# Optimization experiments

Hardware: AMD Instinct MI355X
Metric: run time of the kernel (lower is better)

The kernel has to match this reference:

```python
import jax, jax.numpy as jnp
import numpy as np

DIM = 320
D_STATE = 32
D_CONV = 4
EXPAND = 2
HEADDIM = 80
D_INNER = EXPAND * DIM          # 640
NHEADS = D_INNER // HEADDIM     # 8
NGROUPS = 1
CONV_DIM = D_INNER + 2 * NGROUPS * D_STATE          # 704
D_IN_PROJ = 2 * D_INNER + 2 * NGROUPS * D_STATE + NHEADS  # 1352
PATCH = (16, 16, 16)
NUM_PT_EMB = 2


def setup_inputs() -> dict:
    key = jax.random.key(0)
    ks = jax.random.split(key, 16)
    B, Np = 4, 8
    x = jax.random.normal(ks[0], (B, DIM) + PATCH, dtype=jnp.float32)
    point_coords = jax.random.uniform(ks[1], (B, Np, 3), dtype=jnp.float32) * jnp.asarray(PATCH, jnp.float32)
    point_labels = jax.random.randint(ks[2], (B, Np), 0, 2)
    return {
        "x": x,
        "point_coords": point_coords,
        "ln_w": jnp.ones((DIM,), jnp.float32),
        "ln_b": jnp.zeros((DIM,), jnp.float32),
        "in_proj_w": jax.random.normal(ks[3], (D_IN_PROJ, DIM), jnp.float32) * 0.02,
        "conv_w": jax.random.normal(ks[4], (CONV_DIM, 1, D_CONV), jnp.float32) * 0.2,
        "conv_b": jax.random.normal(ks[5], (CONV_DIM,), jnp.float32) * 0.02,
        "dt_bias": jax.random.uniform(ks[6], (NHEADS,), jnp.float32, 0.0, 0.1),
        "A_log": jnp.log(jax.random.uniform(ks[7], (NHEADS,), jnp.float32, 1.0, 16.0)),
        "Dp": jnp.ones((NHEADS,), jnp.float32),
        "rms_w": jnp.ones((D_INNER,), jnp.float32),
        "out_proj_w": jax.random.normal(ks[8], (DIM, D_INNER), jnp.float32) * 0.02,
        "pe_gauss": jax.random.normal(ks[9], (3, DIM // 2), jnp.float32),
        "point_embed": jax.random.normal(ks[10], (NUM_PT_EMB, DIM), jnp.float32) * 0.02,
        "not_a_point": jax.random.normal(ks[11], (DIM,), jnp.float32) * 0.02,
        "point_labels": point_labels,
    }


def _forward(x, point_coords, ln_w, ln_b, in_proj_w, conv_w, conv_b, dt_bias,
             A_log, Dp, rms_w, out_proj_w, pe_gauss, point_embed, not_a_point,
             point_labels):
    B, C = x.shape[:2]
    img_dims = x.shape[2:]
    n_tokens = int(np.prod(img_dims))
    xf = x.reshape(B, C, n_tokens).transpose(0, 2, 1)  # (B, T, C)

    # ---- PointEncoder (SAM-style random Fourier positional embedding) ----
    pc = point_coords / jnp.asarray(PATCH, x.dtype)     # normalize to [0,1]
    pc = 2.0 * pc - 1.0
    pe = (2.0 * jnp.pi) * (pc @ pe_gauss)               # (B, Np, DIM/2)
    pemb = jnp.concatenate([jnp.sin(pe), jnp.cos(pe)], axis=-1)  # (B, Np, DIM)
    lbl = point_labels[..., None]
    safe = jnp.clip(point_labels, 0, NUM_PT_EMB - 1)
    pemb = jnp.where(lbl == -1, not_a_point, pemb + point_embed[safe])

    seq = jnp.concatenate([xf, pemb], axis=1)           # (B, L, C)
    L = seq.shape[1]

    # ---- LayerNorm ----
    mu = seq.mean(-1, keepdims=True)
    var = jnp.mean((seq - mu) ** 2, axis=-1, keepdims=True)
    xn = (seq - mu) * jax.lax.rsqrt(var + 1e-5) * ln_w + ln_b

    # ---- Mamba2 ----
    zxbcdt = xn @ in_proj_w.T                            # (B, L, 1352)
    z = zxbcdt[..., :D_INNER]
    xBC = zxbcdt[..., D_INNER:D_INNER + CONV_DIM]
    dt = zxbcdt[..., D_INNER + CONV_DIM:]                # (B, L, H)
    dt = jax.nn.softplus(dt + dt_bias)

    # causal depthwise conv1d over channels
    conv = jax.lax.conv_general_dilated(
        xBC.transpose(0, 2, 1), conv_w, (1,), [(D_CONV - 1, 0)],
        feature_group_count=CONV_DIM,
        dimension_numbers=("NCH", "OIH", "NCH"))
    xBC = jax.nn.silu((conv + conv_b[None, :, None]).transpose(0, 2, 1))

    xs = xBC[..., :D_INNER].reshape(B, L, NHEADS, HEADDIM)
    Bm = xBC[..., D_INNER:D_INNER + D_STATE]             # (B, L, N), ngroups=1
    Cm = xBC[..., D_INNER + D_STATE:]                    # (B, L, N)

    A = -jnp.exp(A_log)                                  # (H,)
    dA = jnp.exp(dt * A)                                 # (B, L, H)

    def step(h, inp):
        dA_t, dt_t, B_t, C_t, x_t = inp
        h = h * dA_t[:, :, None, None] + jnp.einsum('bh,bn,bhp->bhpn', dt_t, B_t, x_t)
        y = jnp.einsum('bhpn,bn->bhp', h, C_t)
        return h, y

    inps = (dA.transpose(1, 0, 2), dt.transpose(1, 0, 2),
            Bm.transpose(1, 0, 2), Cm.transpose(1, 0, 2),
            xs.transpose(1, 0, 2, 3))
    h0 = jnp.zeros((B, NHEADS, HEADDIM, D_STATE), x.dtype)
    _, ys = jax.lax.scan(step, h0, inps)                 # (L, B, H, P)
    y = ys.transpose(1, 0, 2, 3) + xs * Dp[None, None, :, None]
    y = y.reshape(B, L, D_INNER)

    # gated RMSNorm
    y = y * jax.nn.silu(z)
    y = y * jax.lax.rsqrt(jnp.mean(y * y, axis=-1, keepdims=True) + 1e-5) * rms_w
    out = y @ out_proj_w.T                               # (B, L, DIM)

    out = out[:, :n_tokens].transpose(0, 2, 1).reshape(B, C, *img_dims)
    return out


def reference(x, point_coords, ln_w, ln_b, in_proj_w, conv_w, conv_b, dt_bias,
              A_log, Dp, rms_w, out_proj_w, pe_gauss, point_embed, not_a_point,
              point_labels):
    return _forward(x, point_coords, ln_w, ln_b, in_proj_w, conv_w, conv_b,
                    dt_bias, A_log, Dp, rms_w, out_proj_w, pe_gauss,
                    point_embed, not_a_point, point_labels)
```

## Files before the change

kernel.cpp:

```cpp
#include <hip/hip_runtime.h>
#include <math.h>

#define BQ 4
#define LQ 4104
#define NTQ 4096
#define CDIM 320
#define DIP 1352
#define DI 640
#define CONVD 704
#define NH 8
#define HD 80
#define DS 32
#define MQ (BQ*LQ)
#define QC 64
#define NC 65

typedef __attribute__((ext_vector_type(8))) short bf16x8;
typedef __attribute__((ext_vector_type(4))) float f32x4;

__device__ __forceinline__ unsigned short f2bf(float f){
  union { float f; unsigned u; } v; v.f = f;
  unsigned r = v.u + 0x7FFFu + ((v.u >> 16) & 1u);
  return (unsigned short)(r >> 16);
}
__device__ __forceinline__ float bf2f(unsigned short u){
  union { unsigned u; float f; } v; v.u = ((unsigned)u) << 16;
  return v.f;
}
__device__ __forceinline__ float warp_sum(float v){
  #pragma unroll
  for (int o = 32; o; o >>= 1) v += __shfl_xor(v, o);
  return v;
}
__device__ __forceinline__ void gload16(const unsigned short* g, unsigned short* l){
  __builtin_amdgcn_global_load_lds(
      (const __attribute__((address_space(1))) unsigned int*)g,
      (__attribute__((address_space(3))) unsigned int*)l, 16, 0, 0);
}
__device__ __forceinline__ int swz64(int p, int i){
  return p*QC + (i ^ ((p & 7) << 3));
}

__global__ __launch_bounds__(256) void k_f2bf2(
    const float* __restrict__ s1, unsigned short* __restrict__ d1, int n1,
    const float* __restrict__ s2, unsigned short* __restrict__ d2, int n2)
{
  int i = blockIdx.x*256 + threadIdx.x;
  if (i < n1) d1[i] = f2bf(s1[i]);
  else if (i - n1 < n2) d2[i - n1] = f2bf(s2[i - n1]);
}

__global__ __launch_bounds__(256) void k_zero(float* __restrict__ p, int n)
{
  int i = blockIdx.x*256 + threadIdx.x;
  if (i < n) p[i] = 0.f;
}

__global__ __launch_bounds__(256) void k_stats(
    const float* __restrict__ x, float* __restrict__ muS, float* __restrict__ s2S)
{
  int b = blockIdx.z;
  int cs0 = blockIdx.y * 40;
  int tok = blockIdx.x*256 + threadIdx.x;
  const float* xb = x + ((size_t)b*CDIM)*NTQ;
  float s = 0.f, s2 = 0.f;
  #pragma unroll 8
  for (int c = cs0; c < cs0 + 40; c++) {
    float v = xb[(size_t)c*NTQ + tok];
    s += v; s2 = fmaf(v, v, s2);
  }
  atomicAdd(&muS[b*NTQ + tok], s);
  atomicAdd(&s2S[b*NTQ + tok], s2);
}

__global__ __launch_bounds__(256) void k_norm_t(
    const float* __restrict__ x, const float* __restrict__ muS,
    const float* __restrict__ s2S, const float* __restrict__ lnw,
    const float* __restrict__ lnb, unsigned short* __restrict__ xnh)
{
  int b = blockIdx.z;
  int c0 = blockIdx.y * 64;
  int t0 = blockIdx.x * 64;
  int t = threadIdx.x;
  int lt = t & 63, cg = t >> 6;
  const float* xb = x + ((size_t)b*CDIM)*NTQ;

  __shared__ unsigned short T[64][72];
  __shared__ float muL[64], rsL[64];
  if (t < 64) {
    float s  = muS[b*NTQ + t0 + t];
    float s2 = s2S[b*NTQ + t0 + t];
    float mu = s*(1.0f/CDIM);
    muL[t] = mu;
    rsL[t] = rsqrtf(s2*(1.0f/CDIM) - mu*mu + 1e-5f);
  }
  __syncthreads();
  float mu = muL[lt], rs = rsL[lt];
  #pragma unroll
  for (int c = cg; c < 64; c += 4) {
    float v = xb[(size_t)(c0+c)*NTQ + t0 + lt];
    T[lt][c] = f2bf((v - mu)*rs*lnw[c0+c] + lnb[c0+c]);
  }
  __syncthreads();
  #pragma unroll
  for (int i = 0; i < 4; i++) {
    int idx = t + 256*i;
    int tok = idx >> 4, cq = idx & 15;
    *(uint2*)&xnh[((size_t)(b*LQ) + t0 + tok)*CDIM + c0 + cq*4] =
        *(const uint2*)&T[tok][cq*4];
  }
}

__global__ __launch_bounds__(320) void k_pt_ln(
    const float* __restrict__ pcoords, const float* __restrict__ lnw,
    const float* __restrict__ lnb, const float* __restrict__ pgauss,
    const float* __restrict__ pemb_w, const float* __restrict__ nap,
    const int* __restrict__ plabels, unsigned short* __restrict__ xnh)
{
  int j = blockIdx.x, b = blockIdx.y;
  int c = threadIdx.x;
  int f = (c < 160) ? c : c - 160;
  float p0 = pcoords[(b*8+j)*3+0]*(2.0f/16.0f) - 1.0f;
  float p1 = pcoords[(b*8+j)*3+1]*(2.0f/16.0f) - 1.0f;
  float p2 = pcoords[(b*8+j)*3+2]*(2.0f/16.0f) - 1.0f;
  float pe = 6.283185307179586f*(p0*pgauss[f] + p1*pgauss[160+f] + p2*pgauss[320+f]);
  float pv = (c < 160) ? sinf(pe) : cosf(pe);
  int lab = plabels[b*8+j];
  float val;
  if (lab == -1) val = nap[c];
  else {
    int safe = lab < 0 ? 0 : (lab > 1 ? 1 : lab);
    val = pv + pemb_w[safe*CDIM + c];
  }
  float s  = warp_sum(val);
  float s2 = warp_sum(val*val);
  __shared__ float r1[5], r2[5];
  int w = threadIdx.x >> 6, lane = threadIdx.x & 63;
  if (lane == 0) { r1[w] = s; r2[w] = s2; }
  __syncthreads();
  float ts = 0.f, ts2 = 0.f;
  #pragma unroll
  for (int i = 0; i < 5; i++) { ts += r1[i]; ts2 += r2[i]; }
  float mu  = ts * (1.0f/CDIM);
  float var = ts2 * (1.0f/CDIM) - mu*mu;
  float rsig = rsqrtf(var + 1e-5f);
  xnh[((size_t)b*LQ + NTQ + j)*CDIM + c] = f2bf((val - mu)*rsig*lnw[c] + lnb[c]);
}

__global__ __launch_bounds__(256) void k_gemm1_mfma(
    const unsigned short* __restrict__ Abf, const unsigned short* __restrict__ Wbf,
    unsigned short* __restrict__ zxh, float* __restrict__ dtraw)
{
  __shared__ unsigned short As[128*32];
  __shared__ unsigned short Bs[128*32];
  int id = blockIdx.x;
  int xcd = id & 7, pos = id >> 3;
  const int q = 177, r = 3;
  int swz = (xcd < r ? xcd*(q+1) : r*(q+1) + (xcd-r)*q) + pos;
  int m0 = (swz / 11) * 128;
  int n0 = (swz % 11) * 128;
  int tid = threadIdx.x;
  int lane = tid & 63, wid = tid >> 6;
  int wr = wid >> 1, wc = wid & 1;
  int fr = lane & 15, fq = lane >> 4;

  int srow = lane >> 2;
  int scol = (lane & 3) * 8;

  f32x4 acc[4][4] = {};
  for (int k0 = 0; k0 < CDIM; k0 += 32) {
    #pragma unroll
    for (int i = 0; i < 2; i++) {
      int seg = wid + i*4;
      int rowA = seg*16 + srow;
      int ga = m0 + rowA; if (ga > MQ-1) ga = MQ-1;
      gload16(Abf + (size_t)ga*CDIM + k0 + scol, &As[seg*512]);
      int gb = n0 + rowA; if (gb > DIP-1) gb = DIP-1;
      gload16(Wbf + (size_t)gb*CDIM + k0 + scol, &Bs[seg*512]);
    }
    __syncthreads();
    bf16x8 fa[4], fb[4];
    #pragma unroll
    for (int i = 0; i < 4; i++) {
      fa[i] = *(const bf16x8*)&As[(wr*64 + i*16 + fr)*32 + fq*8];
      fb[i] = *(const bf16x8*)&Bs[(wc*64 + i*16 + fr)*32 + fq*8];
    }
    #pragma unroll
    for (int i = 0; i < 4; i++)
      #pragma unroll
      for (int j = 0; j < 4; j++)
        acc[i][j] = __builtin_amdgcn_mfma_f32_16x16x32_bf16(fa[i], fb[j], acc[i][j], 0, 0, 0);
    __syncthreads();
  }
  #pragma unroll
  for (int i = 0; i < 4; i++) {
    #pragma unroll
    for (int j = 0; j < 4; j++) {
      #pragma unroll
      for (int rr = 0; rr < 4; rr++) {
        int grow = m0 + wr*64 + i*16 + fq*4 + rr;
        int gcol = n0 + wc*64 + j*16 + fr;
        if (grow < MQ && gcol < DIP) {
          float v = acc[i][j][rr];
          zxh[(size_t)grow*DIP + gcol] = f2bf(v);
          if (gcol >= DI + CONVD)
            dtraw[(size_t)grow*NH + (gcol - (DI + CONVD))] = v;
        }
      }
    }
  }
}

__global__ __launch_bounds__(256) void k_conv(
    const unsigned short* __restrict__ zxh, const float* __restrict__ cw,
    const float* __restrict__ cb, unsigned short* __restrict__ xcb)
{
  const int nC4 = CONVD/4;
  int gid = blockIdx.x*256 + threadIdx.x;
  if (gid >= (MQ/8)*nC4) return;
  int c4 = gid % nC4;
  int mb = gid / nC4;
  int m0 = mb*8;
  int l0 = m0 % LQ;
  int c0 = c4*4;
  float4 cbv = *(const float4*)(cb + c0);
  float4 w0 = *(const float4*)(cw + (c0+0)*4);
  float4 w1 = *(const float4*)(cw + (c0+1)*4);
  float4 w2 = *(const float4*)(cw + (c0+2)*4);
  float4 w3 = *(const float4*)(cw + (c0+3)*4);
  const float* wp[4] = {(const float*)&w0, (const float*)&w1,
                        (const float*)&w2, (const float*)&w3};
  float vals[11][4];
  #pragma unroll
  for (int r = 0; r < 11; r++) {
    int ls = l0 - 3 + r;
    uint2 u = make_uint2(0,0);
    if (ls >= 0)
      u = *(const uint2*)(zxh + (size_t)(m0-3+r)*DIP + DI + c0);
    vals[r][0] = bf2f((unsigned short)(u.x & 0xffff));
    vals[r][1] = bf2f((unsigned short)(u.x >> 16));
    vals[r][2] = bf2f((unsigned short)(u.y & 0xffff));
    vals[r][3] = bf2f((unsigned short)(u.y >> 16));
  }
  const float* cbp = (const float*)&cbv;
  #pragma unroll
  for (int u = 0; u < 8; u++) {
    unsigned short o[4];
    #pragma unroll
    for (int ch = 0; ch < 4; ch++) {
      float a = cbp[ch];
      #pragma unroll
      for (int j = 0; j < 4; j++)
        a = fmaf(vals[u+j][ch], wp[ch][j], a);
      o[ch] = f2bf(a / (1.f + __expf(-a)));
    }
    *(uint2*)(xcb + (size_t)(m0+u)*CONVD + c0) = *(const uint2*)o;
  }
}

__global__ __launch_bounds__(256) void k_cumsum_state(
    const float* __restrict__ dtraw, const float* __restrict__ dt_bias,
    const float* __restrict__ A_log, const unsigned short* __restrict__ xcb,
    float* __restrict__ dtb, float* __restrict__ cs, float* __restrict__ Dc,
    float* __restrict__ Sbuf)
{
  int c = blockIdx.x, h = blockIdx.y, b = blockIdx.z;
  int len = LQ - c*QC; if (len > QC) len = QC;
  int t = threadIdx.x;
  int lane = t & 63, wid = t >> 6;
  int fr = lane & 15, fq = lane >> 4;
  int m0 = b*LQ + c*QC;

  __shared__ unsigned short XT[HD*QC];
  __shared__ unsigned short BwT[DS*QC];
  __shared__ float sm[QC], dtl[QC], ws[QC];

  for (int idx = t; idx < (HD/8)*QC; idx += 256) {
    int pg = idx % 10, i = idx / 10;
    uint4 v = make_uint4(0,0,0,0);
    if (i < len)
      v = *(const uint4*)(xcb + (size_t)(m0+i)*CONVD + h*HD + pg*8);
    union { uint4 u; unsigned short us[8]; } cv; cv.u = v;
    #pragma unroll
    for (int e = 0; e < 8; e++)
      XT[swz64(pg*8+e, i)] = cv.us[e];
  }

  float A = -expf(A_log[h]);
  if (t < QC) {
    float sp = 0.f;
    if (t < len) {
      float v = dtraw[((size_t)(m0+t))*NH + h] + dt_bias[h];
      sp = (v > 20.f) ? v : log1pf(expf(v));
      dtb[((size_t)(m0+t))*NH + h] = sp;
    }
    dtl[t] = sp;
    sm[t] = sp * A;
  }
  __syncthreads();
  for (int off = 1; off < QC; off <<= 1) {
    float v = 0.f;
    if (t < QC && t >= off) v = sm[t-off];
    __syncthreads();
    if (t < QC) sm[t] += v;
    __syncthreads();
  }
  if (t < QC) cs[((size_t)(b*NH+h)*NC + c)*QC + t] = sm[t];
  if (t == len-1) Dc[(b*NH+h)*NC + c] = expf(sm[t]);
  if (t < QC) ws[t] = (t < len) ? __expf(sm[len-1] - sm[t]) * dtl[t] : 0.f;
  __syncthreads();
  for (int idx = t; idx < DS*QC; idx += 256) {
    int n = idx & 31, i = idx >> 5;
    float v = (i < len) ? bf2f(xcb[(size_t)(m0+i)*CONVD + DI + n]) * ws[i] : 0.f;
    BwT[swz64(n, i)] = f2bf(v);
  }
  __syncthreads();

  size_t base = ((size_t)(b*NC + c)*NH + h)*(HD*DS);
  for (int tp = wid; tp < 10; tp += 4) {
    int pi = tp >> 1, ni = tp & 1;
    f32x4 acc = {};
    #pragma unroll
    for (int ks = 0; ks < 2; ks++) {
      bf16x8 fa = *(const bf16x8*)&XT[swz64(pi*16 + fr, ks*32 + fq*8)];
      bf16x8 fb = *(const bf16x8*)&BwT[swz64(ni*16 + fr, ks*32 + fq*8)];
      acc = __builtin_amdgcn_mfma_f32_16x16x32_bf16(fa, fb, acc, 0, 0, 0);
    }
    #pragma unroll
    for (int rr = 0; rr < 4; rr++)
      Sbuf[base + (size_t)(pi*16 + fq*4 + rr)*DS + ni*16 + fr] = acc[rr];
  }
}

__global__ __launch_bounds__(256) void k_state_scan(
    float* __restrict__ Sbuf, const float* __restrict__ Dc,
    float* __restrict__ H0)
{
  int tid = blockIdx.x*256 + threadIdx.x;
  int pn = tid % (HD*DS);
  int bh = tid / (HD*DS);
  int b = bh >> 3, h = bh & 7;
  float hst = 0.f;
  for (int c = 0; c < NC; c++) {
    size_t idx = ((size_t)(b*NC + c)*NH + h)*(HD*DS) + pn;
    float sv = Sbuf[idx];
    H0[idx] = hst;
    hst = hst * Dc[bh*NC + c] + sv;
  }
}

__global__ __launch_bounds__(256) void k_chunk_y_mfma(
    const unsigned short* __restrict__ xcb, const unsigned short* __restrict__ zxh,
    const float* __restrict__ dtb, const float* __restrict__ cs,
    const float* __restrict__ H0, const float* __restrict__ Dp,
    unsigned short* __restrict__ ygb)
{
  int c = blockIdx.x, h = blockIdx.y, b = blockIdx.z;
  int len = LQ - c*QC; if (len > QC) len = QC;
  int t = threadIdx.x;
  int lane = t & 63, wid = t >> 6;
  int fr = lane & 15, fq = lane >> 4;
  int m0 = b*LQ + c*QC;

  __shared__ unsigned short XT[HD*QC];
  __shared__ unsigned short Wt[4*16*32];
  __shared__ float slA[QC], dtlA[QC], elA[QC];

  const float* csb = cs + ((size_t)(b*NH+h)*NC + c)*QC;

  for (int idx = t; idx < (HD/8)*QC; idx += 256) {
    int pg = idx % 10, i = idx / 10;
    uint4 v = make_uint4(0,0,0,0);
    if (i < len)
      v = *(const uint4*)(xcb + (size_t)(m0+i)*CONVD + h*HD + pg*8);
    union { uint4 u; unsigned short us[8]; } cv; cv.u = v;
    #pragma unroll
    for (int e = 0; e < 8; e++)
      XT[swz64(pg*8+e, i)] = cv.us[e];
  }
  if (t < QC) {
    float s = csb[t];
    slA[t] = s;
    elA[t] = __expf(s);
    dtlA[t] = (t < len) ? dtb[((size_t)(m0+t))*NH + h] : 0.f;
  }
  __syncthreads();

  int row16 = wid*16 + fr;
  bf16x8 fa = {};
  if (row16 < len)
    fa = *(const bf16x8*)(xcb + (size_t)(m0+row16)*CONVD + DI + DS + fq*8);

  size_t hb = ((size_t)(b*NC + c)*NH + h)*(HD*DS);
  f32x4 acc[5];
  #pragma unroll
  for (int j = 0; j < 5; j++) {
    int p = j*16 + fr;
    const float* hp = H0 + hb + (size_t)p*DS + fq*8;
    float4 ha = *(const float4*)hp;
    float4 hbv = *(const float4*)(hp + 4);
    bf16x8 fb;
    fb[0]=(short)f2bf(ha.x);  fb[1]=(short)f2bf(ha.y);
    fb[2]=(short)f2bf(ha.z);  fb[3]=(short)f2bf(ha.w);
    fb[4]=(short)f2bf(hbv.x); fb[5]=(short)f2bf(hbv.y);
    fb[6]=(short)f2bf(hbv.z); fb[7]=(short)f2bf(hbv.w);
    f32x4 z = {};
    acc[j] = __builtin_amdgcn_mfma_f32_16x16x32_bf16(fa, fb, z, 0, 0, 0);
  }
  #pragma unroll
  for (int rr = 0; rr < 4; rr++) {
    float el = elA[wid*16 + fq*4 + rr];
    #pragma unroll
    for (int j = 0; j < 5; j++) acc[j][rr] *= el;
  }

  int wbase = wid << 9;
  for (int sc = 0; sc < 2; sc++) {
    int i0 = sc*32;
    #pragma unroll
    for (int jt = 0; jt < 2; jt++) {
      int col = i0 + jt*16 + fr;
      bf16x8 fbv = {};
      if (col < len)
        fbv = *(const bf16x8*)(xcb + (size_t)(m0+col)*CONVD + DI + fq*8);
      float sc_col = slA[col], dt_col = dtlA[col];
      f32x4 z = {};
      f32x4 g = __builtin_amdgcn_mfma_f32_16x16x32_bf16(fa, fbv, z, 0, 0, 0);
      #pragma unroll
      for (int rr = 0; rr < 4; rr++) {
        int lr = fq*4 + rr;
        int row = wid*16 + lr;
        float v = 0.f;
        if (col <= row)
          v = g[rr] * __expf(slA[row] - sc_col) * dt_col;
        int lc = jt*16 + fr;
        int slot = (lc >> 3) ^ (lr & 3);
        Wt[wbase + (lr<<5) + (slot<<3) + (lc&7)] = f2bf(v);
      }
    }
    bf16x8 wa = *(const bf16x8*)&Wt[wbase + (fr<<5) + ((fq ^ (fr&3))<<3)];
    #pragma unroll
    for (int j = 0; j < 5; j++) {
      int p = j*16 + fr;
      bf16x8 xb = *(const bf16x8*)&XT[swz64(p, i0 + fq*8)];
      acc[j] = __builtin_amdgcn_mfma_f32_16x16x32_bf16(wa, xb, acc[j], 0, 0, 0);
    }
  }

  float dpv = Dp[h];
  #pragma unroll
  for (int rr = 0; rr < 4; rr++) {
    int l = wid*16 + fq*4 + rr;
    if (l >= len) continue;
    size_t m = m0 + l;
    #pragma unroll
    for (int j = 0; j < 5; j++) {
      int p = j*16 + fr;
      int cc = h*HD + p;
      float xv = bf2f(XT[swz64(p, l)]);
      float y = acc[j][rr] + xv*dpv;
      float zv = bf2f(zxh[m*DIP + cc]);
      y *= zv / (1.f + __expf(-zv));
      ygb[m*DI + cc] = f2bf(y);
    }
  }
}

__global__ __launch_bounds__(256) void k_rms_scale(
    unsigned short* __restrict__ ygb, const float* __restrict__ rsw)
{
  int t = threadIdx.x;
  int grp = t >> 5;
  int gl = t & 31;
  size_t m = (size_t)blockIdx.x*8 + grp;
  unsigned short* row = ygb + m*DI;
  float v[5][4];
  float ss = 0.f;
  #pragma unroll
  for (int k = 0; k < 5; k++) {
    uint2 u = *(const uint2*)(row + (gl + 32*k)*4);
    v[k][0] = bf2f((unsigned short)(u.x & 0xffff));
    v[k][1] = bf2f((unsigned short)(u.x >> 16));
    v[k][2] = bf2f((unsigned short)(u.y & 0xffff));
    v[k][3] = bf2f((unsigned short)(u.y >> 16));
    ss += v[k][0]*v[k][0] + v[k][1]*v[k][1] + v[k][2]*v[k][2] + v[k][3]*v[k][3];
  }
  #pragma unroll
  for (int o = 16; o; o >>= 1) ss += __shfl_xor(ss, o, 32);
  float rsv = rsqrtf(ss*(1.0f/DI) + 1e-5f);
  #pragma unroll
  for (int k = 0; k < 5; k++) {
    float4 wv = *(const float4*)(rsw + (gl + 32*k)*4);
    unsigned short o4[4];
    o4[0] = f2bf(v[k][0]*rsv*wv.x);
    o4[1] = f2bf(v[k][1]*rsv*wv.y);
    o4[2] = f2bf(v[k][2]*rsv*wv.z);
    o4[3] = f2bf(v[k][3]*rsv*wv.w);
    *(uint2*)(row + (gl + 32*k)*4) = *(const uint2*)o4;
  }
}

__global__ __launch_bounds__(256) void k_gemm2_mfma(
    const unsigned short* __restrict__ W2h, const unsigned short* __restrict__ Ygh,
    float* __restrict__ out)
{
  __shared__ unsigned short As[128*32];
  __shared__ unsigned short Bs[128*32];
  int id = blockIdx.x;
  int xcd = id & 7, pos = id >> 3;
  const int q = 48, r = 3;
  int swz = (xcd < r ? xcd*(q+1) : r*(q+1) + (xcd-r)*q) + pos;
  int c0 = (swz % 3) * 128;
  int t0 = (swz / 3) * 128;
  int tid = threadIdx.x;
  int lane = tid & 63, wid = tid >> 6;
  int wr = wid >> 1, wc = wid & 1;
  int fr = lane & 15, fq = lane >> 4;

  int srow = lane >> 2;
  int scol = (lane & 3) * 8;

  f32x4 acc[4][4] = {};
  for (int k0 = 0; k0 < DI; k0 += 32) {
    #pragma unroll
    for (int i = 0; i < 2; i++) {
      int seg = wid + i*4;
      int rowA = seg*16 + srow;
      int ga = c0 + rowA; if (ga > CDIM-1) ga = CDIM-1;
      gload16(W2h + (size_t)ga*DI + k0 + scol, &As[seg*512]);
      int gb = t0 + rowA; if (gb > MQ-1) gb = MQ-1;
      gload16(Ygh + (size_t)gb*DI + k0 + scol, &Bs[seg*512]);
    }
    __syncthreads();
    bf16x8 fa[4], fb[4];
    #pragma unroll
    for (int i = 0; i < 4; i++) {
      fa[i] = *(const bf16x8*)&As[(wr*64 + i*16 + fr)*32 + fq*8];
      fb[i] = *(const bf16x8*)&Bs[(wc*64 + i*16 + fr)*32 + fq*8];
    }
    #pragma unroll
    for (int i = 0; i < 4; i++)
      #pragma unroll
      for (int j = 0; j < 4; j++)
        acc[i][j] = __builtin_amdgcn_mfma_f32_16x16x32_bf16(fa[i], fb[j], acc[i][j], 0, 0, 0);
    __syncthreads();
  }
  #pragma unroll
  for (int i = 0; i < 4; i++) {
    #pragma unroll
    for (int j = 0; j < 4; j++) {
      #pragma unroll
      for (int rr = 0; rr < 4; rr++) {
        int ch  = c0 + wr*64 + i*16 + fq*4 + rr;
        int tok = t0 + wc*64 + j*16 + fr;
        if (ch < CDIM && tok < MQ) {
          int b = tok / LQ, l = tok % LQ;
          if (l < NTQ)
            out[((size_t)(b*CDIM + ch))*NTQ + l] = acc[i][j][rr];
        }
      }
    }
  }
}

extern "C" void kernel_launch(void* const* d_in, const int* in_sizes, int n_in,
                              void* d_out, int out_size, void* d_ws, size_t ws_size,
                              hipStream_t stream)
{
  const float* x       = (const float*)d_in[0];
  const float* pc      = (const float*)d_in[1];
  const float* lnw     = (const float*)d_in[2];
  const float* lnb     = (const float*)d_in[3];
  const float* w1      = (const float*)d_in[4];
  const float* cw      = (const float*)d_in[5];
  const float* cb      = (const float*)d_in[6];
  const float* dt_bias = (const float*)d_in[7];
  const float* A_log   = (const float*)d_in[8];
  const float* Dp      = (const float*)d_in[9];
  const float* rsw     = (const float*)d_in[10];
  const float* w2      = (const float*)d_in[11];
  const float* pg      = (const float*)d_in[12];
  const float* pew     = (const float*)d_in[13];
  const float* nap     = (const float*)d_in[14];
  const int*   plab    = (const int*)d_in[15];
  float* out = (float*)d_out;

  unsigned short* xnh  = (unsigned short*)d_ws;
  unsigned short* zxh  = xnh + (size_t)MQ*CDIM;
  float* dtraw = (float*)(zxh + (size_t)MQ*DIP);
  unsigned short* xcb  = (unsigned short*)(dtraw + (size_t)MQ*NH);
  float* dtb = (float*)(xcb + (size_t)MQ*CONVD);
  float* cs  = dtb + (size_t)MQ*NH;
  float* Dc  = cs  + (size_t)BQ*NH*NC*QC;
  float* Sb  = Dc  + (size_t)BQ*NH*NC;
  float* H0  = Sb;
  unsigned short* ygb = (unsigned short*)(Sb + (size_t)BQ*NC*NH*HD*DS);
  unsigned short* w1h = ygb + (size_t)MQ*DI;
  unsigned short* w2h = w1h + (size_t)DIP*CDIM;
  float* muS = (float*)(w2h + (size_t)CDIM*DI);
  float* s2S = muS + (size_t)BQ*NTQ;

  k_f2bf2<<<(DIP*CDIM + CDIM*DI + 255)/256, 256, 0, stream>>>(
      w1, w1h, DIP*CDIM, w2, w2h, CDIM*DI);
  k_zero<<<(2*BQ*NTQ + 255)/256, 256, 0, stream>>>(muS, 2*BQ*NTQ);
  dim3 gs(NTQ/256, 8, BQ);
  k_stats<<<gs, 256, 0, stream>>>(x, muS, s2S);
  dim3 gn(NTQ/64, CDIM/64, BQ);
  k_norm_t<<<gn, 256, 0, stream>>>(x, muS, s2S, lnw, lnb, xnh);
  dim3 gp(8, BQ);
  k_pt_ln<<<gp, 320, 0, stream>>>(pc, lnw, lnb, pg, pew, nap, plab, xnh);
  k_gemm1_mfma<<<129*11, 256, 0, stream>>>(xnh, w1h, zxh, dtraw);
  k_conv<<<((MQ/8)*(CONVD/4) + 255)/256, 256, 0, stream>>>(zxh, cw, cb, xcb);
  dim3 gc(NC, NH, BQ);
  k_cumsum_state<<<gc, 256, 0, stream>>>(dtraw, dt_bias, A_log, xcb, dtb, cs, Dc, Sb);
  k_state_scan<<<(BQ*NH*HD*DS)/256, 256, 0, stream>>>(Sb, Dc, H0);
  k_chunk_y_mfma<<<gc, 256, 0, stream>>>(xcb, zxh, dtb, cs, H0, Dp, ygb);
  k_rms_scale<<<MQ/8, 256, 0, stream>>>(ygb, rsw);
  k_gemm2_mfma<<<129*3, 256, 0, stream>>>(w2h, ygb, out);
}
```

Before: 167.0 us.

## Double-buffer GEMM LDS tiles, drop stats atomics, vectorize weight cast, warp-shuffle cumsum

Both MFMA GEMMs now use two LDS buffers, so the async global-to-LDS load of the next K tile overlaps the MFMAs on the current one. The layernorm statistics kernel writes per-slice partial sums that the norm kernel adds up, which removes the atomics and the zeroing kernel. The weight bf16 conversion is vectorized with float4 loads. The chunk cumsum uses a warp shuffle scan in place of a shared-memory scan with many barriers. Doubling the LDS footprint may reduce occupancy, and the partial-sum buffer is larger than the old one and needs more workspace.

```diff
diff --git a/kernel.cpp b/kernel.cpp
--- a/kernel.cpp
+++ b/kernel.cpp
@@ -41,26 +41,29 @@
   return p*QC + (i ^ ((p & 7) << 3));
 }
 
-__global__ __launch_bounds__(256) void k_f2bf2(
-    const float* __restrict__ s1, unsigned short* __restrict__ d1, int n1,
-    const float* __restrict__ s2, unsigned short* __restrict__ d2, int n2)
-{
-  int i = blockIdx.x*256 + threadIdx.x;
-  if (i < n1) d1[i] = f2bf(s1[i]);
-  else if (i - n1 < n2) d2[i - n1] = f2bf(s2[i - n1]);
-}
-
-__global__ __launch_bounds__(256) void k_zero(float* __restrict__ p, int n)
-{
-  int i = blockIdx.x*256 + threadIdx.x;
-  if (i < n) p[i] = 0.f;
+__global__ __launch_bounds__(256) void k_f2bf4(
+    const float* __restrict__ s1, unsigned short* __restrict__ d1, int n14,
+    const float* __restrict__ s2, unsigned short* __restrict__ d2, int n24)
+{
+  int i4 = blockIdx.x*256 + threadIdx.x;
+  if (i4 < n14) {
+    float4 v = ((const float4*)s1)[i4];
+    unsigned short o[4] = {f2bf(v.x), f2bf(v.y), f2bf(v.z), f2bf(v.w)};
+    *(uint2*)&d1[i4*4] = *(const uint2*)o;
+  } else if (i4 - n14 < n24) {
+    int j = i4 - n14;
+    float4 v = ((const float4*)s2)[j];
+    unsigned short o[4] = {f2bf(v.x), f2bf(v.y), f2bf(v.z), f2bf(v.w)};
+    *(uint2*)&d2[j*4] = *(const uint2*)o;
+  }
 }
 
 __global__ __launch_bounds__(256) void k_stats(
-    const float* __restrict__ x, float* __restrict__ muS, float* __restrict__ s2S)
+    const float* __restrict__ x, float* __restrict__ muP, float* __restrict__ s2P)
 {
   int b = blockIdx.z;
-  int cs0 = blockIdx.y * 40;
+  int sl = blockIdx.y;
+  int cs0 = sl * 40;
   int tok = blockIdx.x*256 + threadIdx.x;
   const float* xb = x + ((size_t)b*CDIM)*NTQ;
   float s = 0.f, s2 = 0.f;
@@ -69,13 +72,13 @@
     float v = xb[(size_t)c*NTQ + tok];
     s += v; s2 = fmaf(v, v, s2);
   }
-  atomicAdd(&muS[b*NTQ + tok], s);
-  atomicAdd(&s2S[b*NTQ + tok], s2);
+  muP[((size_t)sl*BQ + b)*NTQ + tok] = s;
+  s2P[((size_t)sl*BQ + b)*NTQ + tok] = s2;
 }
 
 __global__ __launch_bounds__(256) void k_norm_t(
-    const float* __restrict__ x, const float* __restrict__ muS,
-    const float* __restrict__ s2S, const float* __restrict__ lnw,
+    const float* __restrict__ x, const float* __restrict__ muP,
+    const float* __restrict__ s2P, const float* __restrict__ lnw,
     const float* __restrict__ lnb, unsigned short* __restrict__ xnh)
 {
   int b = blockIdx.z;
@@ -88,8 +91,12 @@
   __shared__ unsigned short T[64][72];
   __shared__ float muL[64], rsL[64];
   if (t < 64) {
-    float s  = muS[b*NTQ + t0 + t];
-    float s2 = s2S[b*NTQ + t0 + t];
+    float s = 0.f, s2 = 0.f;
+    #pragma unroll
+    for (int sl = 0; sl < 8; sl++) {
+      s  += muP[((size_t)sl*BQ + b)*NTQ + t0 + t];
+      s2 += s2P[((size_t)sl*BQ + b)*NTQ + t0 + t];
+    }
     float mu = s*(1.0f/CDIM);
     muL[t] = mu;
     rsL[t] = rsqrtf(s2*(1.0f/CDIM) - mu*mu + 1e-5f);
@@ -151,8 +158,8 @@
     const unsigned short* __restrict__ Abf, const unsigned short* __restrict__ Wbf,
     unsigned short* __restrict__ zxh, float* __restrict__ dtraw)
 {
-  __shared__ unsigned short As[128*32];
-  __shared__ unsigned short Bs[128*32];
+  __shared__ unsigned short As[2][128*32];
+  __shared__ unsigned short Bs[2][128*32];
   int id = blockIdx.x;
   int xcd = id & 7, pos = id >> 3;
   const int q = 177, r = 3;
@@ -163,35 +170,49 @@
   int lane = tid & 63, wid = tid >> 6;
   int wr = wid >> 1, wc = wid & 1;
   int fr = lane & 15, fq = lane >> 4;
-
   int srow = lane >> 2;
   int scol = (lane & 3) * 8;
 
+#define G1_STAGE(buf, kk)                                                   \
+  {                                                                         \
+    _Pragma("unroll")                                                       \
+    for (int i = 0; i < 2; i++) {                                           \
+      int seg = wid + i*4;                                                  \
+      int rowA = seg*16 + srow;                                             \
+      int ga = m0 + rowA; if (ga > MQ-1) ga = MQ-1;                         \
+      gload16(Abf + (size_t)ga*CDIM + (kk) + scol, &As[buf][seg*512]);      \
+      int gb = n0 + rowA; if (gb > DIP-1) gb = DIP-1;                       \
+      gload16(Wbf + (size_t)gb*CDIM + (kk) + scol, &Bs[buf][seg*512]);      \
+    }                                                                       \
+  }
+
+#define G1_COMPUTE(buf)                                                     \
+  {                                                                         \
+    bf16x8 fa[4], fb[4];                                                    \
+    _Pragma("unroll")                                                       \
+    for (int i = 0; i < 4; i++) {                                           \
+      fa[i] = *(const bf16x8*)&As[buf][(wr*64 + i*16 + fr)*32 + fq*8];      \
+      fb[i] = *(const bf16x8*)&Bs[buf][(wc*64 + i*16 + fr)*32 + fq*8];      \
+    }                                                                       \
+    _Pragma("unroll")                                                       \
+    for (int i = 0; i < 4; i++)                                             \
+      _Pragma("unroll")                                                     \
+      for (int j = 0; j < 4; j++)                                           \
+        acc[i][j] = __builtin_amdgcn_mfma_f32_16x16x32_bf16(fa[i], fb[j], acc[i][j], 0, 0, 0); \
+  }
+
   f32x4 acc[4][4] = {};
-  for (int k0 = 0; k0 < CDIM; k0 += 32) {
-    #pragma unroll
-    for (int i = 0; i < 2; i++) {
-      int seg = wid + i*4;
-      int rowA = seg*16 + srow;
-      int ga = m0 + rowA; if (ga > MQ-1) ga = MQ-1;
-      gload16(Abf + (size_t)ga*CDIM + k0 + scol, &As[seg*512]);
-      int gb = n0 + rowA; if (gb > DIP-1) gb = DIP-1;
-      gload16(Wbf + (size_t)gb*CDIM + k0 + scol, &Bs[seg*512]);
-    }
+  G1_STAGE(0, 0);
+  __syncthreads();
+  int cur = 0;
+  for (int k0 = 32; k0 < CDIM; k0 += 32) {
+    G1_STAGE(cur^1, k0);
+    G1_COMPUTE(cur);
     __syncthreads();
-    bf16x8 fa[4], fb[4];
-    #pragma unroll
-    for (int i = 0; i < 4; i++) {
-      fa[i] = *(const bf16x8*)&As[(wr*64 + i*16 + fr)*32 + fq*8];
-      fb[i] = *(const bf16x8*)&Bs[(wc*64 + i*16 + fr)*32 + fq*8];
-    }
-    #pragma unroll
-    for (int i = 0; i < 4; i++)
-      #pragma unroll
-      for (int j = 0; j < 4; j++)
-        acc[i][j] = __builtin_amdgcn_mfma_f32_16x16x32_bf16(fa[i], fb[j], acc[i][j], 0, 0, 0);
-    __syncthreads();
-  }
+    cur ^= 1;
+  }
+  G1_COMPUTE(cur);
+
   #pragma unroll
   for (int i = 0; i < 4; i++) {
     #pragma unroll
@@ -273,7 +294,7 @@
 
   __shared__ unsigned short XT[HD*QC];
   __shared__ unsigned short BwT[DS*QC];
-  __shared__ float sm[QC], dtl[QC], ws[QC];
+  __shared__ float ws[QC];
 
   for (int idx = t; idx < (HD/8)*QC; idx += 256) {
     int pg = idx % 10, i = idx / 10;
@@ -286,28 +307,25 @@
       XT[swz64(pg*8+e, i)] = cv.us[e];
   }
 
-  float A = -expf(A_log[h]);
   if (t < QC) {
+    float A = -expf(A_log[h]);
     float sp = 0.f;
     if (t < len) {
       float v = dtraw[((size_t)(m0+t))*NH + h] + dt_bias[h];
       sp = (v > 20.f) ? v : log1pf(expf(v));
       dtb[((size_t)(m0+t))*NH + h] = sp;
     }
-    dtl[t] = sp;
-    sm[t] = sp * A;
-  }
-  __syncthreads();
-  for (int off = 1; off < QC; off <<= 1) {
-    float v = 0.f;
-    if (t < QC && t >= off) v = sm[t-off];
-    __syncthreads();
-    if (t < QC) sm[t] += v;
-    __syncthreads();
-  }
-  if (t < QC) cs[((size_t)(b*NH+h)*NC + c)*QC + t] = sm[t];
-  if (t == len-1) Dc[(b*NH+h)*NC + c] = expf(sm[t]);
-  if (t < QC) ws[t] = (t < len) ? __expf(sm[len-1] - sm[t]) * dtl[t] : 0.f;
+    float a = sp * A;
+    #pragma unroll
+    for (int off = 1; off < 64; off <<= 1) {
+      float pv = __shfl_up(a, off, 64);
+      if (t >= off) a += pv;
+    }
+    cs[((size_t)(b*NH+h)*NC + c)*QC + t] = a;
+    if (t == len-1) Dc[(b*NH+h)*NC + c] = expf(a);
+    float aEnd = __shfl(a, len-1, 64);
+    ws[t] = (t < len) ? __expf(aEnd - a) * sp : 0.f;
+  }
   __syncthreads();
   for (int idx = t; idx < DS*QC; idx += 256) {
     int n = idx & 31, i = idx >> 5;
@@ -504,8 +522,8 @@
     const unsigned short* __restrict__ W2h, const unsigned short* __restrict__ Ygh,
     float* __restrict__ out)
 {
-  __shared__ unsigned short As[128*32];
-  __shared__ unsigned short Bs[128*32];
+  __shared__ unsigned short As[2][128*32];
+  __shared__ unsigned short Bs[2][128*32];
   int id = blockIdx.x;
   int xcd = id & 7, pos = id >> 3;
   const int q = 48, r = 3;
@@ -516,35 +534,49 @@
   int lane = tid & 63, wid = tid >> 6;
   int wr = wid >> 1, wc = wid & 1;
   int fr = lane & 15, fq = lane >> 4;
-
   int srow = lane >> 2;
   int scol = (lane & 3) * 8;
 
+#define G2_STAGE(buf, kk)                                                   \
+  {                                                                         \
+    _Pragma("unroll")                                                       \
+    for (int i = 0; i < 2; i++) {                                           \
+      int seg = wid + i*4;                                                  \
+      int rowA = seg*16 + srow;                                             \
+      int ga = c0 + rowA; if (ga > CDIM-1) ga = CDIM-1;                     \
+      gload16(W2h + (size_t)ga*DI + (kk) + scol, &As[buf][seg*512]);        \
+      int gb = t0 + rowA; if (gb > MQ-1) gb = MQ-1;                         \
+      gload16(Ygh + (size_t)gb*DI + (kk) + scol, &Bs[buf][seg*512]);        \
+    }                                                                       \
+  }
+
+#define G2_COMPUTE(buf)                                                     \
+  {                                                                         \
+    bf16x8 fa[4], fb[4];                                                    \
+    _Pragma("unroll")                                                       \
+    for (int i = 0; i < 4; i++) {                                           \
+      fa[i] = *(const bf16x8*)&As[buf][(wr*64 + i*16 + fr)*32 + fq*8];      \
+      fb[i] = *(const bf16x8*)&Bs[buf][(wc*64 + i*16 + fr)*32 + fq*8];      \
+    }                                                                       \
+    _Pragma("unroll")                                                       \
+    for (int i = 0; i < 4; i++)                                             \
+      _Pragma("unroll")                                                     \
+      for (int j = 0; j < 4; j++)                                           \
+        acc[i][j] = __builtin_amdgcn_mfma_f32_16x16x32_bf16(fa[i], fb[j], acc[i][j], 0, 0, 0); \
+  }
+
   f32x4 acc[4][4] = {};
-  for (int k0 = 0; k0 < DI; k0 += 32) {
-    #pragma unroll
-    for (int i = 0; i < 2; i++) {
-      int seg = wid + i*4;
-      int rowA = seg*16 + srow;
-      int ga = c0 + rowA; if (ga > CDIM-1) ga = CDIM-1;
-      gload16(W2h + (size_t)ga*DI + k0 + scol, &As[seg*512]);
-      int gb = t0 + rowA; if (gb > MQ-1) gb = MQ-1;
-      gload16(Ygh + (size_t)gb*DI + k0 + scol, &Bs[seg*512]);
-    }
+  G2_STAGE(0, 0);
+  __syncthreads();
+  int cur = 0;
+  for (int k0 = 32; k0 < DI; k0 += 32) {
+    G2_STAGE(cur^1, k0);
+    G2_COMPUTE(cur);
     __syncthreads();
-    bf16x8 fa[4], fb[4];
-    #pragma unroll
-    for (int i = 0; i < 4; i++) {
-      fa[i] = *(const bf16x8*)&As[(wr*64 + i*16 + fr)*32 + fq*8];
-      fb[i] = *(const bf16x8*)&Bs[(wc*64 + i*16 + fr)*32 + fq*8];
-    }
-    #pragma unroll
-    for (int i = 0; i < 4; i++)
-      #pragma unroll
-      for (int j = 0; j < 4; j++)
-        acc[i][j] = __builtin_amdgcn_mfma_f32_16x16x32_bf16(fa[i], fb[j], acc[i][j], 0, 0, 0);
-    __syncthreads();
-  }
+    cur ^= 1;
+  }
+  G2_COMPUTE(cur);
+
   #pragma unroll
   for (int i = 0; i < 4; i++) {
     #pragma unroll
@@ -597,16 +629,15 @@
   unsigned short* ygb = (unsigned short*)(Sb + (size_t)BQ*NC*NH*HD*DS);
   unsigned short* w1h = ygb + (size_t)MQ*DI;
   unsigned short* w2h = w1h + (size_t)DIP*CDIM;
-  float* muS = (float*)(w2h + (size_t)CDIM*DI);
-  float* s2S = muS + (size_t)BQ*NTQ;
-
-  k_f2bf2<<<(DIP*CDIM + CDIM*DI + 255)/256, 256, 0, stream>>>(
-      w1, w1h, DIP*CDIM, w2, w2h, CDIM*DI);
-  k_zero<<<(2*BQ*NTQ + 255)/256, 256, 0, stream>>>(muS, 2*BQ*NTQ);
+  float* muP = (float*)(w2h + (size_t)CDIM*DI);
+  float* s2P = muP + (size_t)8*BQ*NTQ;
+
+  k_f2bf4<<<((DIP*CDIM + CDIM*DI)/4 + 255)/256, 256, 0, stream>>>(
+      w1, w1h, DIP*CDIM/4, w2, w2h, CDIM*DI/4);
   dim3 gs(NTQ/256, 8, BQ);
-  k_stats<<<gs, 256, 0, stream>>>(x, muS, s2S);
+  k_stats<<<gs, 256, 0, stream>>>(x, muP, s2P);
   dim3 gn(NTQ/64, CDIM/64, BQ);
-  k_norm_t<<<gn, 256, 0, stream>>>(x, muS, s2S, lnw, lnb, xnh);
+  k_norm_t<<<gn, 256, 0, stream>>>(x, muP, s2P, lnw, lnb, xnh);
   dim3 gp(8, BQ);
   k_pt_ln<<<gp, 320, 0, stream>>>(pc, lnw, lnb, pg, pew, nap, plab, xnh);
   k_gemm1_mfma<<<129*11, 256, 0, stream>>>(xnh, w1h, zxh, dtraw);
```

Measured after the change: 159.4 us. 1.05x faster.
